# Kernel optimization log

Measured on AMD Instinct MI355X. Metric: run time of the kernel, lower is better.

## Reference

```python
import jax, jax.numpy as jnp
import numpy as np

K = 3  # neighbors for knn_interpolate


def _knn_interpolate(x, pos, pos_skip, B, k):
    """PyG knn_interpolate with equal-sized batches.
    x: [N_coarse, C], pos: [N_coarse, 3], pos_skip: [N_fine, 3].
    """
    C = x.shape[1]
    xb = x.reshape(B, -1, C)          # [B, nc, C]
    pb = pos.reshape(B, -1, 3)        # [B, nc, 3]
    qb = pos_skip.reshape(B, -1, 3)   # [B, nf, 3]

    def per_cloud(xf, pf, qf):
        # squared distances [nf, nc]
        d2 = jnp.sum((qf[:, None, :] - pf[None, :, :]) ** 2, axis=-1)
        neg_d2k, idx = jax.lax.top_k(-d2, k)          # k smallest distances
        d2k = -neg_d2k                                # [nf, k]
        w = 1.0 / jnp.clip(d2k, 1e-16)                # inverse-distance weights
        w = jax.lax.stop_gradient(w)                  # PyG computes weights under no_grad
        feats = xf[idx]                               # [nf, k, C] gather
        return jnp.sum(w[..., None] * feats, axis=1) / jnp.sum(w, axis=1, keepdims=True)

    y = jax.vmap(per_cloud)(xb, pb, qb)               # [B, nf, C]
    return y.reshape(-1, C)


def setup_inputs() -> dict:
    key = jax.random.key(0)
    ks = jax.random.split(key, 8)
    B, n_coarse, n_fine = 16, 1024, 4096
    C_in, C_skip, C_mid, C_out = 256, 128, 256, 256
    x = jax.random.normal(ks[0], (B * n_coarse, C_in), jnp.float32)
    pos = jax.random.uniform(ks[1], (B * n_coarse, 3), jnp.float32)
    x_skip = jax.random.normal(ks[2], (B * n_fine, C_skip), jnp.float32)
    pos_skip = jax.random.uniform(ks[3], (B * n_fine, 3), jnp.float32)
    batch = jnp.repeat(jnp.arange(B, dtype=jnp.int64), n_coarse)
    batch_skip = jnp.repeat(jnp.arange(B, dtype=jnp.int64), n_fine)
    seed_idx = jnp.arange(B * n_coarse, dtype=jnp.int64)
    seed_idx_skip = jnp.arange(B * n_fine, dtype=jnp.int64)
    W1 = jax.random.normal(ks[4], (C_in + C_skip, C_mid), jnp.float32) * 0.05
    b1 = jnp.zeros((C_mid,), jnp.float32)
    W2 = jax.random.normal(ks[5], (C_mid, C_out), jnp.float32) * 0.05
    b2 = jnp.zeros((C_out,), jnp.float32)
    return {"x": x, "pos": pos, "batch": batch, "seed_idx": seed_idx,
            "x_skip": x_skip, "pos_skip": pos_skip, "batch_skip": batch_skip,
            "seed_idx_skip": seed_idx_skip, "W1": W1, "b1": b1, "W2": W2, "b2": b2}


def reference(x, pos, batch, seed_idx, x_skip, pos_skip, batch_skip, seed_idx_skip,
              W1, b1, W2, b2):
    B = int(batch[-1]) + 1  # equal-sized contiguous clouds
    y = _knn_interpolate(x, pos, pos_skip, B, K)      # [N_fine, C_in]
    h = jnp.concatenate([y, x_skip], axis=1)          # [N_fine, C_in+C_skip]
    h = jax.nn.relu(h @ W1 + b1)                      # MLP layer 1
    out = jax.nn.relu(h @ W2 + b2)                    # MLP layer 2
    return (out, pos_skip, batch_skip)
```

## Files before the change

kernel.cpp:

```cpp
#include <hip/hip_runtime.h>
#include <hip/hip_bf16.h>

#define NB    16
#define NC    1024
#define NF    4096
#define NFINE (NB*NF)
#define CIN   256
#define CSKIP 128
#define KH    (CIN+CSKIP)
#define CMID  256
#define COUT  256

typedef __attribute__((ext_vector_type(8))) short short8;
typedef __attribute__((ext_vector_type(4))) float f32x4;
typedef __attribute__((ext_vector_type(4))) unsigned int u32x4;

__device__ __forceinline__ float bf2f(short s) {
    return __uint_as_float(((unsigned)(unsigned short)s) << 16);
}

__global__ __launch_bounds__(256)
void bin_kernel(const float* __restrict__ pos,
                float* __restrict__ gp,
                int* __restrict__ gcs)
{
    __shared__ int cnt[512];
    __shared__ float lx[NC], ly[NC], lz[NC];
    __shared__ short lcell[NC];
    const int b = blockIdx.x, t = threadIdx.x;
    for (int i = t; i < 512; i += 256) cnt[i] = 0;
    __syncthreads();
    const float* pc = pos + (size_t)b*NC*3;
    #pragma unroll
    for (int u = 0; u < 4; ++u) {
        int i = t + u*256;
        float x = pc[3*i+0], y = pc[3*i+1], z = pc[3*i+2];
        int cx = min(7, (int)(x*8.0f));
        int cy = min(7, (int)(y*8.0f));
        int cz = min(7, (int)(z*8.0f));
        int c = (cz*8 + cy)*8 + cx;
        lx[i] = x; ly[i] = y; lz[i] = z; lcell[i] = (short)c;
        atomicAdd(&cnt[c], 1);
    }
    __syncthreads();
    if (t < 64) {
        int v[8]; int s = 0;
        #pragma unroll
        for (int u = 0; u < 8; ++u) { v[u] = cnt[t*8+u]; s += v[u]; }
        int pfx = s;
        #pragma unroll
        for (int m = 1; m < 64; m <<= 1) {
            int o = __shfl_up(pfx, m);
            if (t >= m) pfx += o;
        }
        pfx -= s;
        #pragma unroll
        for (int u = 0; u < 8; ++u) {
            gcs[b*513 + t*8+u] = pfx;
            cnt[t*8+u] = pfx;
            pfx += v[u];
        }
        if (t == 63) gcs[b*513 + 512] = NC;
    }
    __syncthreads();
    #pragma unroll
    for (int u = 0; u < 4; ++u) {
        int i = t + u*256;
        int c = lcell[i];
        int dst = atomicAdd(&cnt[c], 1);
        f32x4 v; v[0] = lx[i]; v[1] = ly[i]; v[2] = lz[i]; v[3] = __int_as_float(i);
        *(f32x4*)&gp[(size_t)(b*NC + dst)*4] = v;
    }
}

#define KQPB 64

#define INS(d, j) do {                                        \
    bool c2 = (d) < dB, c1 = (d) < dA, c0 = (d) < d0;         \
    dB = c1 ? dA : (c2 ? (d) : dB);                           \
    iB = c1 ? iA : (c2 ? (j) : iB);                           \
    dA = c0 ? d0 : (c1 ? (d) : dA);                           \
    iA = c0 ? i0 : (c1 ? (j) : iA);                           \
    d0 = c0 ? (d) : d0;                                       \
    i0 = c0 ? (j) : i0;                                       \
} while (0)

#define SCAN(JS, JE) for (int j = (JS) + g; j < (JE); j += 8) {        \
    const f32x4 p = *(const f32x4*)&pp[j][0];                          \
    float fx = qx - p[0], fy = qy - p[1], fz = qz - p[2];              \
    float dd = fx*fx + fy*fy + fz*fz;                                  \
    INS(dd, j);                                                        \
}

#define MERGE8() do {                                                          \
    _Pragma("unroll")                                                          \
    for (int mm = 1; mm < 8; mm <<= 1) {                                       \
        float e0 = __shfl_xor(d0, mm), e1 = __shfl_xor(dA, mm), e2 = __shfl_xor(dB, mm); \
        int   f0 = __shfl_xor(i0, mm), f1 = __shfl_xor(iA, mm), f2 = __shfl_xor(iB, mm); \
        INS(e0, f0); INS(e1, f1); INS(e2, f2);                                 \
    }                                                                          \
} while (0)

__global__ __launch_bounds__(512)
void knn_grid_kernel(const float* __restrict__ pos_skip,
                     const float* __restrict__ gp,
                     const int* __restrict__ gcs,
                     int* __restrict__ widx, float* __restrict__ wval)
{
    __shared__ __align__(16) float pp[NC][4];
    __shared__ unsigned short cs[513];
    const int bpc = NF/KQPB;
    const int b  = blockIdx.x / bpc;
    const int qb = blockIdx.x % bpc;
    const int t  = threadIdx.x;
    for (int i = t; i < NC; i += 512)
        *(f32x4*)&pp[i][0] = *(const f32x4*)&gp[(size_t)(b*NC + i)*4];
    for (int i = t; i < 513; i += 512) cs[i] = (unsigned short)gcs[b*513 + i];
    __syncthreads();

    const int g  = t & 7;
    const int ql = t >> 3;
    const int q  = b*NF + qb*KQPB + ql;
    const float qx = pos_skip[(size_t)q*3+0];
    const float qy = pos_skip[(size_t)q*3+1];
    const float qz = pos_skip[(size_t)q*3+2];
    const int cx = min(7, (int)(qx*8.0f));
    const int cy = min(7, (int)(qy*8.0f));
    const int cz = min(7, (int)(qz*8.0f));

    float d0 = 3.0e38f, dA = 3.0e38f, dB = 3.0e38f;
    int   i0 = 0,       iA = 0,       iB = 0;

    const int xlo = max(cx-1,0), xhi = min(cx+1,7);
    const int ylo = max(cy-1,0), yhi = min(cy+1,7);
    const int zlo = max(cz-1,0), zhi = min(cz+1,7);
    #pragma unroll
    for (int r = 0; r < 9; ++r) {
        const int z = cz - 1 + r/3;
        const int y = cy - 1 + r%3;
        const bool ok = ((unsigned)z < 8u) & ((unsigned)y < 8u);
        const int rb = (z*8 + y)*8;
        int js = 0, je = 0;
        if (ok) { js = cs[rb + xlo]; je = cs[rb + xhi + 1]; }
        SCAN(js, je);
    }
    MERGE8();

    float m1 = 3.0e38f;
    if (xlo > 0) m1 = fminf(m1, qx - xlo*0.125f);
    if (xhi < 7) m1 = fminf(m1, (xhi+1)*0.125f - qx);
    if (ylo > 0) m1 = fminf(m1, qy - ylo*0.125f);
    if (yhi < 7) m1 = fminf(m1, (yhi+1)*0.125f - qy);
    if (zlo > 0) m1 = fminf(m1, qz - zlo*0.125f);
    if (zhi < 7) m1 = fminf(m1, (zhi+1)*0.125f - qz);

    if (dB > m1*m1) {
        const float s0 = d0, s1 = dA, s2 = dB;
        const int   t0 = i0, t1 = iA, t2 = iB;
        d0 = dA = dB = 3.0e38f; i0 = iA = iB = 0;

        const int xlo2 = max(cx-2,0), xhi2 = min(cx+2,7);
        const int ylo2 = max(cy-2,0), yhi2 = min(cy+2,7);
        const int zlo2 = max(cz-2,0), zhi2 = min(cz+2,7);
        for (int z = zlo2; z <= zhi2; ++z)
        for (int y = ylo2; y <= yhi2; ++y) {
            const int rb = (z*8 + y)*8;
            const bool inner_zy = (z >= zlo && z <= zhi && y >= ylo && y <= yhi);
            int jsA, jeA, jsB, jeB;
            if (inner_zy) {
                jsA = cs[rb + xlo2]; jeA = cs[rb + xlo];
                jsB = cs[rb + xhi + 1]; jeB = cs[rb + xhi2 + 1];
            } else {
                jsA = cs[rb + xlo2]; jeA = cs[rb + xhi2 + 1];
                jsB = 0; jeB = 0;
            }
            SCAN(jsA, jeA);
            SCAN(jsB, jeB);
        }
        MERGE8();
        INS(s0, t0); INS(s1, t1); INS(s2, t2);

        float m2 = 3.0e38f;
        if (xlo2 > 0) m2 = fminf(m2, qx - xlo2*0.125f);
        if (xhi2 < 7) m2 = fminf(m2, (xhi2+1)*0.125f - qx);
        if (ylo2 > 0) m2 = fminf(m2, qy - ylo2*0.125f);
        if (yhi2 < 7) m2 = fminf(m2, (yhi2+1)*0.125f - qy);
        if (zlo2 > 0) m2 = fminf(m2, qz - zlo2*0.125f);
        if (zhi2 < 7) m2 = fminf(m2, (zhi2+1)*0.125f - qz);
        if (dB > m2*m2) {
            const float u0 = d0, u1 = dA, u2 = dB;
            const int   v0 = i0, v1 = iA, v2 = iB;
            d0 = dA = dB = 3.0e38f; i0 = iA = iB = 0;
            for (int j = g; j < NC; j += 8) {
                const f32x4 p = *(const f32x4*)&pp[j][0];
                int pcx = min(7, (int)(p[0]*8.0f));
                int pcy = min(7, (int)(p[1]*8.0f));
                int pcz = min(7, (int)(p[2]*8.0f));
                if (pcx >= xlo2 && pcx <= xhi2 && pcy >= ylo2 && pcy <= yhi2 &&
                    pcz >= zlo2 && pcz <= zhi2) continue;
                float fx = qx - p[0], fy = qy - p[1], fz = qz - p[2];
                float dd = fx*fx + fy*fy + fz*fz;
                INS(dd, j);
            }
            MERGE8();
            INS(u0, v0); INS(u1, v1); INS(u2, v2);
        }
    }

    if (g == 0) {
        const int o0 = __float_as_int(pp[i0][3]);
        const int o1 = __float_as_int(pp[iA][3]);
        const int o2 = __float_as_int(pp[iB][3]);
        float w0 = 1.0f / fmaxf(d0, 1e-16f);
        float w1 = 1.0f / fmaxf(dA, 1e-16f);
        float w2 = 1.0f / fmaxf(dB, 1e-16f);
        float inv = 1.0f / (w0 + w1 + w2);
        widx[q*3+0] = b*NC + o0;  wval[q*3+0] = w0*inv;
        widx[q*3+1] = b*NC + o1;  wval[q*3+1] = w1*inv;
        widx[q*3+2] = b*NC + o2;  wval[q*3+2] = w2*inv;
    }
}

__global__ __launch_bounds__(256)
void prep_weights(const float* __restrict__ W1, const float* __restrict__ W2,
                  __hip_bfloat16* __restrict__ W1at,
                  __hip_bfloat16* __restrict__ W1bt,
                  __hip_bfloat16* __restrict__ W2t)
{
    int e = blockIdx.x*256 + threadIdx.x;
    if (e < CMID*CIN) {
        int n = e / CIN, k = e % CIN;
        W1at[e] = __float2bfloat16(W1[(size_t)k*CMID + n]);
    }
    int e2 = e - CMID*CIN;
    if (e2 >= 0 && e2 < CMID*CSKIP) {
        int n = e2 / CSKIP, k = e2 % CSKIP;
        W1bt[e2] = __float2bfloat16(W1[(size_t)(CIN + k)*CMID + n]);
    }
    int e3 = e - CMID*CIN - CMID*CSKIP;
    if (e3 >= 0 && e3 < COUT*CMID) {
        int n = e3 / CMID, k = e3 % CMID;
        W2t[e3] = __float2bfloat16(W2[(size_t)k*COUT + n]);
    }
}

__global__ __launch_bounds__(512, 2)
void gemmZ_kernel(const float* __restrict__ x,
                  const __hip_bfloat16* __restrict__ W1at,
                  __hip_bfloat16* __restrict__ Z)
{
    __shared__ __align__(16) short As[64][64];
    __shared__ __align__(16) short Bs[256][64];
    const int m0 = blockIdx.x * 64;

    const int t = threadIdx.x;
    const int wave = t >> 6, lane = t & 63;
    const int wm = wave >> 2, wn = wave & 3;
    const int rl = lane & 15, kq = lane >> 4;
    const short* Br = (const short*)W1at;

    const int ar = t >> 3;
    const int ac = t & 7;

    f32x4 rA[2];
    u32x4 rB[4];

    #define LOADAZ(K0) do {                                                    \
        const float* p = &x[(size_t)(m0+ar)*CIN + (K0) + ac*8];                \
        rA[0] = *(const f32x4*)p; rA[1] = *(const f32x4*)(p+4);                \
    } while (0)
    #define LOADBZ(K0) do {                                                    \
        _Pragma("unroll")                                                      \
        for (int i = 0; i < 4; ++i) {                                          \
            const int ch = t + i*512;                                          \
            const int rr = ch >> 3, cc = ch & 7;                               \
            rB[i] = *(const u32x4*)&Br[(size_t)rr*CIN + (K0) + cc*8];          \
        }                                                                      \
    } while (0)

    f32x4 acc[2][4] = {};
    LOADAZ(0); LOADBZ(0);

    #pragma unroll
    for (int s = 0; s < 4; ++s) {
        __syncthreads();
        {
            short8 sv;
            #pragma unroll
            for (int u = 0; u < 2; ++u) {
                f32x4 a = rA[u];
                #pragma unroll
                for (int e = 0; e < 4; ++e) {
                    __hip_bfloat16 bb = __float2bfloat16(a[e]);
                    ((short*)&sv)[u*4+e] = *(short*)&bb;
                }
            }
            *(short8*)&As[ar][(ac ^ (ar&7))*8] = sv;
        }
        #pragma unroll
        for (int i = 0; i < 4; ++i) {
            const int ch = t + i*512;
            const int rr = ch >> 3, cc = ch & 7;
            *(u32x4*)&Bs[rr][(cc ^ (rr&7))*8] = rB[i];
        }
        __syncthreads();
        if (s < 3) { LOADAZ((s+1)*64); LOADBZ((s+1)*64); }
        #pragma unroll
        for (int kh = 0; kh < 2; ++kh) {
            const int kc = kh*4 + kq;
            short8 af[2], bf[4];
            #pragma unroll
            for (int mf = 0; mf < 2; ++mf)
                af[mf] = *(const short8*)&As[wm*32 + mf*16 + rl][(kc ^ (rl&7))*8];
            #pragma unroll
            for (int nf = 0; nf < 4; ++nf)
                bf[nf] = *(const short8*)&Bs[wn*64 + nf*16 + rl][(kc ^ (rl&7))*8];
            #pragma unroll
            for (int mf = 0; mf < 2; ++mf)
            #pragma unroll
            for (int nf = 0; nf < 4; ++nf)
                acc[mf][nf] = __builtin_amdgcn_mfma_f32_16x16x32_bf16(af[mf], bf[nf], acc[mf][nf], 0,0,0);
        }
    }
    #undef LOADAZ
    #undef LOADBZ

    #pragma unroll
    for (int mf = 0; mf < 2; ++mf)
    #pragma unroll
    for (int nf = 0; nf < 4; ++nf) {
        const int col = wn*64 + nf*16 + rl;
        #pragma unroll
        for (int i = 0; i < 4; ++i) {
            const int row = m0 + wm*32 + mf*16 + kq*4 + i;
            Z[(size_t)row*CMID + col] = __float2bfloat16(acc[mf][nf][i]);
        }
    }
}

__global__ __launch_bounds__(512, 2)
void g2_fused(const float* __restrict__ x_skip,
              const __hip_bfloat16* __restrict__ W1bt,
              const float* __restrict__ b1,
              const __hip_bfloat16* __restrict__ Z,
              const int* __restrict__ widx,
              const float* __restrict__ wval,
              const __hip_bfloat16* __restrict__ W2t,
              const float* __restrict__ b2,
              float* __restrict__ out)
{
    __shared__ __align__(16) short As[64][64];
    __shared__ __align__(16) short Bs[256][64];
    __shared__ __align__(16) short Hs[64][256];
    __shared__ int   jjs[64][3];
    __shared__ float wws[64][3];
    const int nwg = gridDim.x;
    const int tile = (blockIdx.x & 7)*(nwg >> 3) + (blockIdx.x >> 3);
    const int m0 = tile * 64;

    const int t = threadIdx.x;
    const int wave = t >> 6, lane = t & 63;
    const int wm = wave >> 2, wn = wave & 3;
    const int rl = lane & 15, kq = lane >> 4;
    const short* Bg = (const short*)W1bt;
    const short* B2r = (const short*)W2t;
    const short* Zr = (const short*)Z;

    const int ar = t >> 3;
    const int ac = t & 7;

    if (t < 192) {
        jjs[t/3][t%3] = widx[(m0 + t/3)*3 + t%3];
        wws[t/3][t%3] = wval[(m0 + t/3)*3 + t%3];
    }

    f32x4 rA[2];
    u32x4 rB[4];

    #define LOADAG(K0) do {                                                    \
        const float* p = &x_skip[(size_t)(m0+ar)*CSKIP + (K0) + ac*8];         \
        rA[0] = *(const f32x4*)p; rA[1] = *(const f32x4*)(p+4);                \
    } while (0)
    #define LOADBX(BP, KT, K0) do {                                            \
        _Pragma("unroll")                                                      \
        for (int i = 0; i < 4; ++i) {                                          \
            const int ch = t + i*512;                                          \
            const int rr = ch >> 3, cc = ch & 7;                               \
            rB[i] = *(const u32x4*)&(BP)[(size_t)rr*(KT) + (K0) + cc*8];       \
        }                                                                      \
    } while (0)
    #define STAGE_A() do {                                                     \
        short8 sv;                                                             \
        _Pragma("unroll")                                                      \
        for (int u = 0; u < 2; ++u) {                                          \
            f32x4 a = rA[u];                                                   \
            _Pragma("unroll")                                                  \
            for (int e = 0; e < 4; ++e) {                                      \
                __hip_bfloat16 bb = __float2bfloat16(a[e]);                    \
                ((short*)&sv)[u*4+e] = *(short*)&bb;                           \
            }                                                                  \
        }                                                                      \
        *(short8*)&As[ar][(ac ^ (ar&7))*8] = sv;                               \
    } while (0)
    #define STAGE_B() do {                                                     \
        _Pragma("unroll")                                                      \
        for (int i = 0; i < 4; ++i) {                                          \
            const int ch = t + i*512;                                          \
            const int rr = ch >> 3, cc = ch & 7;                               \
            *(u32x4*)&Bs[rr][(cc ^ (rr&7))*8] = rB[i];                         \
        }                                                                      \
    } while (0)

    f32x4 acc[2][4] = {};
    #define MFMA1() do {                                                       \
        _Pragma("unroll")                                                      \
        for (int kh = 0; kh < 2; ++kh) {                                       \
            const int kc = kh*4 + kq;                                          \
            short8 af[2], bf[4];                                               \
            _Pragma("unroll")                                                  \
            for (int mf = 0; mf < 2; ++mf)                                     \
                af[mf] = *(const short8*)&As[wm*32 + mf*16 + rl][(kc ^ (rl&7))*8]; \
            _Pragma("unroll")                                                  \
            for (int nf = 0; nf < 4; ++nf)                                     \
                bf[nf] = *(const short8*)&Bs[wn*64 + nf*16 + rl][(kc ^ (rl&7))*8]; \
            _Pragma("unroll")                                                  \
            for (int mf = 0; mf < 2; ++mf)                                     \
            _Pragma("unroll")                                                  \
            for (int nf = 0; nf < 4; ++nf)                                     \
                acc[mf][nf] = __builtin_amdgcn_mfma_f32_16x16x32_bf16(af[mf], bf[nf], acc[mf][nf], 0,0,0); \
        }                                                                      \
    } while (0)

    LOADAG(0); LOADBX(Bg, CSKIP, 0);
    __syncthreads();
    STAGE_A(); STAGE_B();
    __syncthreads();
    LOADAG(64); LOADBX(Bg, CSKIP, 64);
    MFMA1();
    __syncthreads();
    STAGE_A(); STAGE_B();
    __syncthreads();
    LOADBX(B2r, CMID, 0);
    MFMA1();

    #pragma unroll
    for (int mf = 0; mf < 2; ++mf)
    #pragma unroll
    for (int nf = 0; nf < 4; ++nf) {
        const int col = wn*64 + nf*16 + rl;
        const float bv = b1[col];
        #pragma unroll
        for (int i = 0; i < 4; ++i) {
            const int row = wm*32 + mf*16 + kq*4 + i;
            float v = acc[mf][nf][i] + bv;
            __hip_bfloat16 bb = __float2bfloat16(v);
            Hs[row][((col >> 3) ^ (row & 7))*8 + (col & 7)] = *(short*)&bb;
        }
    }
    __syncthreads();

    #pragma unroll
    for (int u = 0; u < 4; ++u) {
        const int ch = t + u*512;
        const int row = ch >> 5;
        const int cc  = ch & 31;
        const int c   = cc * 8;
        const int j0 = jjs[row][0], j1 = jjs[row][1], j2 = jjs[row][2];
        const float w0 = wws[row][0], w1 = wws[row][1], w2 = wws[row][2];
        const short8 z0 = *(const short8*)&Zr[(size_t)j0*CMID + c];
        const short8 z1 = *(const short8*)&Zr[(size_t)j1*CMID + c];
        const short8 z2 = *(const short8*)&Zr[(size_t)j2*CMID + c];
        const int slot = (cc ^ (row & 7))*8;
        short8 gchunk = *(const short8*)&Hs[row][slot];
        short8 r;
        #pragma unroll
        for (int e = 0; e < 8; ++e) {
            float v = bf2f(gchunk[e]) + w0*bf2f(z0[e]) + w1*bf2f(z1[e]) + w2*bf2f(z2[e]);
            v = fmaxf(v, 0.0f);
            __hip_bfloat16 bb = __float2bfloat16(v);
            r[e] = *(short*)&bb;
        }
        *(short8*)&Hs[row][slot] = r;
    }

    f32x4 acc2[2][4] = {};
    #define MFMA2(S2) do {                                                     \
        _Pragma("unroll")                                                      \
        for (int kh = 0; kh < 2; ++kh) {                                       \
            const int kcl = kh*4 + kq;                                         \
            const int kca = (S2)*8 + kcl;                                      \
            short8 af[2], bf[4];                                               \
            _Pragma("unroll")                                                  \
            for (int mf = 0; mf < 2; ++mf)                                     \
                af[mf] = *(const short8*)&Hs[wm*32 + mf*16 + rl][(kca ^ (rl&7))*8]; \
            _Pragma("unroll")                                                  \
            for (int nf = 0; nf < 4; ++nf)                                     \
                bf[nf] = *(const short8*)&Bs[wn*64 + nf*16 + rl][(kcl ^ (rl&7))*8]; \
            _Pragma("unroll")                                                  \
            for (int mf = 0; mf < 2; ++mf)                                     \
            _Pragma("unroll")                                                  \
            for (int nf = 0; nf < 4; ++nf)                                     \
                acc2[mf][nf] = __builtin_amdgcn_mfma_f32_16x16x32_bf16(af[mf], bf[nf], acc2[mf][nf], 0,0,0); \
        }                                                                      \
    } while (0)

    __syncthreads();
    STAGE_B();
    __syncthreads();
    LOADBX(B2r, CMID, 64);
    MFMA2(0);
    __syncthreads();
    STAGE_B();
    __syncthreads();
    LOADBX(B2r, CMID, 128);
    MFMA2(1);
    __syncthreads();
    STAGE_B();
    __syncthreads();
    LOADBX(B2r, CMID, 192);
    MFMA2(2);
    __syncthreads();
    STAGE_B();
    __syncthreads();
    MFMA2(3);

    #pragma unroll
    for (int mf = 0; mf < 2; ++mf)
    #pragma unroll
    for (int nf = 0; nf < 4; ++nf) {
        const int col = wn*64 + nf*16 + rl;
        const float bv = b2[col];
        #pragma unroll
        for (int i = 0; i < 4; ++i) {
            const int row = m0 + wm*32 + mf*16 + kq*4 + i;
            out[(size_t)row*COUT + col] = fmaxf(acc2[mf][nf][i] + bv, 0.0f);
        }
    }
    #undef LOADAG
    #undef LOADBX
    #undef STAGE_A
    #undef STAGE_B
    #undef MFMA1
    #undef MFMA2
}

__global__ __launch_bounds__(256)
void tail_kernel(const float* __restrict__ pos_skip, float* __restrict__ out)
{
    int e = blockIdx.x*256 + threadIdx.x;
    if (e < NFINE*3) out[(size_t)NFINE*COUT + e] = pos_skip[e];
    if (e < NFINE)   out[(size_t)NFINE*COUT + (size_t)NFINE*3 + e] = (float)(e / NF);
}

extern "C" void kernel_launch(void* const* d_in, const int* in_sizes, int n_in,
                              void* d_out, int out_size, void* d_ws, size_t ws_size,
                              hipStream_t stream) {
    const float* x        = (const float*)d_in[0];
    const float* pos      = (const float*)d_in[1];
    const float* x_skip   = (const float*)d_in[4];
    const float* pos_skip = (const float*)d_in[5];
    const float* W1       = (const float*)d_in[8];
    const float* b1       = (const float*)d_in[9];
    const float* W2       = (const float*)d_in[10];
    const float* b2       = (const float*)d_in[11];
    float* out = (float*)d_out;
    char* ws = (char*)d_ws;

    int*            widx = (int*)  (ws + 0);
    float*          wval = (float*)(ws + 786432);
    __hip_bfloat16* W1at = (__hip_bfloat16*)(ws + 1572864);
    __hip_bfloat16* W1bt = (__hip_bfloat16*)(ws + 1703936);
    __hip_bfloat16* W2t  = (__hip_bfloat16*)(ws + 1769472);
    float*          gp   = (float*)(ws + 1900544);
    int*            gcs  = (int*)  (ws + 2162688);
    __hip_bfloat16* Z    = (__hip_bfloat16*)(ws + 2195520);

    hipLaunchKernelGGL(bin_kernel, dim3(NB), dim3(256), 0, stream,
                       pos, gp, gcs);
    hipLaunchKernelGGL(knn_grid_kernel, dim3(NB*(NF/KQPB)), dim3(512), 0, stream,
                       pos_skip, gp, gcs, widx, wval);
    hipLaunchKernelGGL(prep_weights, dim3((CMID*CIN + CMID*CSKIP + COUT*CMID + 255)/256), dim3(256), 0, stream,
                       W1, W2, W1at, W1bt, W2t);
    hipLaunchKernelGGL(gemmZ_kernel, dim3((NB*NC)/64), dim3(512), 0, stream,
                       x, W1at, Z);
    hipLaunchKernelGGL(g2_fused, dim3(NFINE/64), dim3(512), 0, stream,
                       x_skip, W1bt, b1, Z, widx, wval, W2t, b2, out);
    hipLaunchKernelGGL(tail_kernel, dim3((NFINE*3 + 255)/256), dim3(256), 0, stream,
                       pos_skip, out);
}
```

Before: 73.40 us.

## Read weight fragments directly from global memory instead of staging through LDS

```diff
diff --git a/kernel.cpp b/kernel.cpp
--- a/kernel.cpp
+++ b/kernel.cpp
@@ -349,8 +349,7 @@
               const float* __restrict__ b2,
               float* __restrict__ out)
 {
-    __shared__ __align__(16) short As[64][64];
-    __shared__ __align__(16) short Bs[256][64];
+    __shared__ __align__(16) short As[64][128];
     __shared__ __align__(16) short Hs[64][256];
     __shared__ int   jjs[64][3];
     __shared__ float wws[64][3];
@@ -362,86 +361,65 @@
     const int wave = t >> 6, lane = t & 63;
     const int wm = wave >> 2, wn = wave & 3;
     const int rl = lane & 15, kq = lane >> 4;
-    const short* Bg = (const short*)W1bt;
+    const short* Bg  = (const short*)W1bt;
     const short* B2r = (const short*)W2t;
-    const short* Zr = (const short*)Z;
+    const short* Zr  = (const short*)Z;
 
     const int ar = t >> 3;
     const int ac = t & 7;
+    const int sw = (ac ^ (ar & 7));
+
+    const float* xs = &x_skip[(size_t)(m0+ar)*CSKIP];
+    f32x4 pa0 = *(const f32x4*)&xs[ac*8];
+    f32x4 pa1 = *(const f32x4*)&xs[ac*8+4];
+    f32x4 pb0 = *(const f32x4*)&xs[64+ac*8];
+    f32x4 pb1 = *(const f32x4*)&xs[64+ac*8+4];
 
     if (t < 192) {
         jjs[t/3][t%3] = widx[(m0 + t/3)*3 + t%3];
         wws[t/3][t%3] = wval[(m0 + t/3)*3 + t%3];
     }
 
-    f32x4 rA[2];
-    u32x4 rB[4];
-
-    #define LOADAG(K0) do {                                                    \
-        const float* p = &x_skip[(size_t)(m0+ar)*CSKIP + (K0) + ac*8];         \
-        rA[0] = *(const f32x4*)p; rA[1] = *(const f32x4*)(p+4);                \
-    } while (0)
-    #define LOADBX(BP, KT, K0) do {                                            \
-        _Pragma("unroll")                                                      \
-        for (int i = 0; i < 4; ++i) {                                          \
-            const int ch = t + i*512;                                          \
-            const int rr = ch >> 3, cc = ch & 7;                               \
-            rB[i] = *(const u32x4*)&(BP)[(size_t)rr*(KT) + (K0) + cc*8];       \
-        }                                                                      \
-    } while (0)
-    #define STAGE_A() do {                                                     \
-        short8 sv;                                                             \
-        _Pragma("unroll")                                                      \
-        for (int u = 0; u < 2; ++u) {                                          \
-            f32x4 a = rA[u];                                                   \
-            _Pragma("unroll")                                                  \
-            for (int e = 0; e < 4; ++e) {                                      \
-                __hip_bfloat16 bb = __float2bfloat16(a[e]);                    \
-                ((short*)&sv)[u*4+e] = *(short*)&bb;                           \
-            }                                                                  \
-        }                                                                      \
-        *(short8*)&As[ar][(ac ^ (ar&7))*8] = sv;                               \
-    } while (0)
-    #define STAGE_B() do {                                                     \
-        _Pragma("unroll")                                                      \
-        for (int i = 0; i < 4; ++i) {                                          \
-            const int ch = t + i*512;                                          \
-            const int rr = ch >> 3, cc = ch & 7;                               \
-            *(u32x4*)&Bs[rr][(cc ^ (rr&7))*8] = rB[i];                         \
-        }                                                                      \
-    } while (0)
+    {
+        short8 sv0, sv1;
+        #pragma unroll
+        for (int u = 0; u < 2; ++u) {
+            f32x4 a = (u == 0) ? pa0 : pa1;
+            f32x4 b = (u == 0) ? pb0 : pb1;
+            #pragma unroll
+            for (int e = 0; e < 4; ++e) {
+                __hip_bfloat16 ba = __float2bfloat16(a[e]);
+                __hip_bfloat16 bb = __float2bfloat16(b[e]);
+                ((short*)&sv0)[u*4+e] = *(short*)&ba;
+                ((short*)&sv1)[u*4+e] = *(short*)&bb;
+            }
+        }
+        *(short8*)&As[ar][sw*8]       = sv0;
+        *(short8*)&As[ar][(8+sw)*8]   = sv1;
+    }
+    __syncthreads();
 
     f32x4 acc[2][4] = {};
-    #define MFMA1() do {                                                       \
-        _Pragma("unroll")                                                      \
-        for (int kh = 0; kh < 2; ++kh) {                                       \
-            const int kc = kh*4 + kq;                                          \
-            short8 af[2], bf[4];                                               \
-            _Pragma("unroll")                                                  \
-            for (int mf = 0; mf < 2; ++mf)                                     \
-                af[mf] = *(const short8*)&As[wm*32 + mf*16 + rl][(kc ^ (rl&7))*8]; \
-            _Pragma("unroll")                                                  \
-            for (int nf = 0; nf < 4; ++nf)                                     \
-                bf[nf] = *(const short8*)&Bs[wn*64 + nf*16 + rl][(kc ^ (rl&7))*8]; \
-            _Pragma("unroll")                                                  \
-            for (int mf = 0; mf < 2; ++mf)                                     \
-            _Pragma("unroll")                                                  \
-            for (int nf = 0; nf < 4; ++nf)                                     \
-                acc[mf][nf] = __builtin_amdgcn_mfma_f32_16x16x32_bf16(af[mf], bf[nf], acc[mf][nf], 0,0,0); \
-        }                                                                      \
-    } while (0)
-
-    LOADAG(0); LOADBX(Bg, CSKIP, 0);
-    __syncthreads();
-    STAGE_A(); STAGE_B();
-    __syncthreads();
-    LOADAG(64); LOADBX(Bg, CSKIP, 64);
-    MFMA1();
-    __syncthreads();
-    STAGE_A(); STAGE_B();
-    __syncthreads();
-    LOADBX(B2r, CMID, 0);
-    MFMA1();
+    #pragma unroll
+    for (int s = 0; s < 2; ++s) {
+        #pragma unroll
+        for (int kh = 0; kh < 2; ++kh) {
+            const int kc = kh*4 + kq;
+            const int kabs = s*64 + kc*8;
+            short8 af[2], bf[4];
+            #pragma unroll
+            for (int mf = 0; mf < 2; ++mf)
+                af[mf] = *(const short8*)&As[wm*32 + mf*16 + rl][(s*8 + (kc ^ (rl&7)))*8];
+            #pragma unroll
+            for (int nf = 0; nf < 4; ++nf)
+                bf[nf] = *(const short8*)&Bg[(size_t)(wn*64 + nf*16 + rl)*CSKIP + kabs];
+            #pragma unroll
+            for (int mf = 0; mf < 2; ++mf)
+            #pragma unroll
+            for (int nf = 0; nf < 4; ++nf)
+                acc[mf][nf] = __builtin_amdgcn_mfma_f32_16x16x32_bf16(af[mf], bf[nf], acc[mf][nf], 0,0,0);
+        }
+    }
 
     #pragma unroll
     for (int mf = 0; mf < 2; ++mf)
@@ -482,47 +460,29 @@
         }
         *(short8*)&Hs[row][slot] = r;
     }
+    __syncthreads();
 
     f32x4 acc2[2][4] = {};
-    #define MFMA2(S2) do {                                                     \
-        _Pragma("unroll")                                                      \
-        for (int kh = 0; kh < 2; ++kh) {                                       \
-            const int kcl = kh*4 + kq;                                         \
-            const int kca = (S2)*8 + kcl;                                      \
-            short8 af[2], bf[4];                                               \
-            _Pragma("unroll")                                                  \
-            for (int mf = 0; mf < 2; ++mf)                                     \
-                af[mf] = *(const short8*)&Hs[wm*32 + mf*16 + rl][(kca ^ (rl&7))*8]; \
-            _Pragma("unroll")                                                  \
-            for (int nf = 0; nf < 4; ++nf)                                     \
-                bf[nf] = *(const short8*)&Bs[wn*64 + nf*16 + rl][(kcl ^ (rl&7))*8]; \
-            _Pragma("unroll")                                                  \
-            for (int mf = 0; mf < 2; ++mf)                                     \
-            _Pragma("unroll")                                                  \
-            for (int nf = 0; nf < 4; ++nf)                                     \
-                acc2[mf][nf] = __builtin_amdgcn_mfma_f32_16x16x32_bf16(af[mf], bf[nf], acc2[mf][nf], 0,0,0); \
-        }                                                                      \
-    } while (0)
-
-    __syncthreads();
-    STAGE_B();
-    __syncthreads();
-    LOADBX(B2r, CMID, 64);
-    MFMA2(0);
-    __syncthreads();
-    STAGE_B();
-    __syncthreads();
-    LOADBX(B2r, CMID, 128);
-    MFMA2(1);
-    __syncthreads();
-    STAGE_B();
-    __syncthreads();
-    LOADBX(B2r, CMID, 192);
-    MFMA2(2);
-    __syncthreads();
-    STAGE_B();
-    __syncthreads();
-    MFMA2(3);
+    #pragma unroll
+    for (int s2 = 0; s2 < 4; ++s2) {
+        #pragma unroll
+        for (int kh = 0; kh < 2; ++kh) {
+            const int kcl = kh*4 + kq;
+            const int kca = s2*8 + kcl;
+            short8 af[2], bf[4];
+            #pragma unroll
+            for (int mf = 0; mf < 2; ++mf)
+                af[mf] = *(const short8*)&Hs[wm*32 + mf*16 + rl][(kca ^ (rl&7))*8];
+            #pragma unroll
+            for (int nf = 0; nf < 4; ++nf)
+                bf[nf] = *(const short8*)&B2r[(size_t)(wn*64 + nf*16 + rl)*CMID + kca*8];
+            #pragma unroll
+            for (int mf = 0; mf < 2; ++mf)
+            #pragma unroll
+            for (int nf = 0; nf < 4; ++nf)
+                acc2[mf][nf] = __builtin_amdgcn_mfma_f32_16x16x32_bf16(af[mf], bf[nf], acc2[mf][nf], 0,0,0);
+        }
+    }
 
     #pragma unroll
     for (int mf = 0; mf < 2; ++mf)
@@ -536,12 +496,6 @@
             out[(size_t)row*COUT + col] = fmaxf(acc2[mf][nf][i] + bv, 0.0f);
         }
     }
-    #undef LOADAG
-    #undef LOADBX
-    #undef STAGE_A
-    #undef STAGE_B
-    #undef MFMA1
-    #undef MFMA2
 }
 
 __global__ __launch_bounds__(256)
```

Measured after the change: 100.8 us. 37.3% more time.
